# Kernel optimization log

Hardware: AMD Instinct MI355X
Metric: run time of the kernel (lower is better)

Reference implementation:

```python
import jax, jax.numpy as jnp
from jax import lax
import numpy as np

B, N = 8, 16384
C = 16            # layer_channels
K = 2             # kernel_size
L = 30            # layer_nums (layer 0 is plain causal conv, 29 gated layers)
AGG = 64          # agregate1x1 out channels
OUT = 256         # output1x1 out channels (8-bit classes)


def causal_conv(x, w, dilation):
    # x: (B, Cin, N), w: (Cout, Cin, K) -> (B, Cout, N), left-padded (causal)
    k = w.shape[-1]
    return lax.conv_general_dilated(
        x, w, window_strides=(1,), padding=[(dilation * (k - 1), 0)],
        rhs_dilation=(dilation,), dimension_numbers=('NCH', 'OIH', 'NCH'))


def setup_inputs() -> dict:
    key = jax.random.key(0)
    ks = jax.random.split(key, 16)
    s = 0.1
    x = jax.random.normal(ks[0], (B, N), dtype=jnp.float32) * 8000.0  # raw 16-bit-ish audio
    lengths = jax.random.randint(ks[1], (B,), N // 2, N, dtype=jnp.int32)
    return {
        'x': x,
        'lengths': lengths,
        'W0': jax.random.normal(ks[2], (C, 1, K), dtype=jnp.float32) * s,
        'b0': jnp.zeros((C,), dtype=jnp.float32),
        'Wf': jax.random.normal(ks[3], (L - 1, C, C, K), dtype=jnp.float32) * s,
        'bf': jnp.zeros((L - 1, C), dtype=jnp.float32),
        'Wg': jax.random.normal(ks[4], (L - 1, C, C, K), dtype=jnp.float32) * s,
        'bg': jnp.zeros((L - 1, C), dtype=jnp.float32),
        'Wr': jax.random.normal(ks[5], (L - 1, C, C), dtype=jnp.float32) * s,
        'br': jnp.zeros((L - 1, C), dtype=jnp.float32),
        'Wa': jax.random.normal(ks[6], (AGG, C), dtype=jnp.float32) * s,
        'ba': jnp.zeros((AGG,), dtype=jnp.float32),
        'Wo': jax.random.normal(ks[7], (OUT, AGG), dtype=jnp.float32) * s,
        'bo': jnp.zeros((OUT,), dtype=jnp.float32),
    }


def reference(x, lengths, W0, b0, Wf, bf, Wg, bg, Wr, br, Wa, ba, Wo, bo):
    inp = (x / 32768.0)[:, None, :]                     # (B,1,N), 65536/2 scaling
    # layer 0: plain causal conv 1 -> C
    h = causal_conv(inp, W0, 1) + b0[:, None]           # (B,C,N)
    skip = h
    inp = inp + h                                       # (B,1,N)+(B,C,N) broadcast
    for i in range(1, L):
        d = 2 ** (i % 10)
        j = i - 1
        f = jnp.tanh(causal_conv(inp, Wf[j], d) + bf[j][:, None])
        g = jax.nn.sigmoid(causal_conv(inp, Wg[j], d) + bg[j][:, None])
        z = f * g                                       # gated activation
        out = jnp.einsum('oc,bcn->bon', Wr[j], z) + br[j][:, None]
        skip = skip + out                               # skip-sum accumulation
        inp = inp + out                                 # residual
    a = jnp.einsum('oc,bcn->bon', Wa, jax.nn.relu(skip)) + ba[:, None]
    o = jnp.einsum('oc,bcn->bon', Wo, jax.nn.relu(a)) + bo[:, None]
    logp = jax.nn.log_softmax(o, axis=1)                # (B,OUT,N)
    mask = (jnp.arange(N) < lengths[:, None])[:, None, :].astype(logp.dtype)
    return logp * mask
```

## Files before the change

kernel.cpp:

```cpp
#include <hip/hip_runtime.h>
#include <hip/hip_bf16.h>

#define NN 16384
#define NC 16
#define NPOSTOT 131072
#define NLAY 29
#define TOUT 256
#define LSTR 24

typedef float4 f4;
typedef short bf16x8 __attribute__((ext_vector_type(8)));
typedef float f32x4 __attribute__((ext_vector_type(4)));

#define OFF_WF 0
#define OFF_WG (NLAY * 512)
#define OFF_WR (2 * NLAY * 512)
#define OFF_WA (3 * NLAY * 512)
#define OFF_WO (3 * NLAY * 512 + 2048)
#define PK_TOT (OFF_WO + 16384)

static __device__ __forceinline__ short to_bf16(float f) {
    __hip_bfloat16 h = __float2bfloat16(f);
    short s;
    __builtin_memcpy(&s, &h, 2);
    return s;
}
static __device__ __forceinline__ float from_bf16(short s) {
    unsigned int u = ((unsigned int)(unsigned short)s) << 16;
    float f;
    __builtin_memcpy(&f, &u, 4);
    return f;
}

__global__ __launch_bounds__(256) void prepack_k(
    const float* __restrict__ Wf, const float* __restrict__ Wg,
    const float* __restrict__ Wr, const float* __restrict__ Wa,
    const float* __restrict__ Wo, short* __restrict__ pk)
{
    const int i = blockIdx.x * 256 + threadIdx.x;
    if (i >= PK_TOT) return;
    float val;
    if (i < OFF_WG) {
        const int j = i >> 9, r = i & 511, l = r >> 3, j8 = r & 7;
        const int o = l & 15, h = l >> 4;
        const int k = h * 8 + j8, tap = k >> 4, c = k & 15;
        val = Wf[((j * 16 + o) * 16 + c) * 2 + tap];
    } else if (i < OFF_WA) {
        const int i2 = i - OFF_WG;
        if (i2 < NLAY * 512) {
            const int j = i2 >> 9, r = i2 & 511, l = r >> 3, j8 = r & 7;
            const int o = l & 15, h = l >> 4;
            const int k = h * 8 + j8, tap = k >> 4, c = k & 15;
            val = Wg[((j * 16 + o) * 16 + c) * 2 + tap];
        } else {
            const int i3 = i2 - NLAY * 512;
            const int j = i3 >> 9, r = i3 & 511, l = r >> 3, j8 = r & 7;
            const int o = l & 15, h = l >> 4;
            val = (j8 < 4) ? Wr[j * 256 + o * 16 + h * 4 + j8] : 0.0f;
        }
    } else if (i < OFF_WO) {
        const int i2 = i - OFF_WA;
        const int mt = i2 >> 9, r = i2 & 511, l = r >> 3, j8 = r & 7;
        const int og = mt * 16 + (l & 15), h = l >> 4;
        const int k = h * 8 + j8;
        val = (k < 16) ? Wa[og * 16 + k] : 0.0f;
    } else {
        const int i2 = i - OFF_WO;
        const int qt = i2 >> 10, hf = (i2 >> 9) & 1, r = i2 & 511;
        const int l = r >> 3, j8 = r & 7;
        const int q = qt * 16 + (l & 15), h = l >> 4;
        const int kg = hf * 32 + (j8 >> 2) * 16 + h * 4 + (j8 & 3);
        val = Wo[q * 64 + kg];
    }
    pk[i] = to_bf16(val);
}

static __device__ __forceinline__ f32x4 gated_core2(
    bf16x8 bx, bf16x8 af_, bf16x8 ag_, bf16x8 ar_,
    f32x4 cf, f32x4 cg, f32x4 cr)
{
    const f32x4 fp = __builtin_amdgcn_mfma_f32_16x16x32_bf16(af_, bx, cf, 0, 0, 0);
    const f32x4 gp = __builtin_amdgcn_mfma_f32_16x16x32_bf16(ag_, bx, cg, 0, 0, 0);

    bf16x8 bz;
#pragma unroll
    for (int r = 0; r < 4; ++r) {
        const float ef = __expf(2.0f * fminf(fp[r], 43.0f));
        const float eg = __expf(-gp[r]);
        const float den = fmaf(ef, eg, ef) + (eg + 1.0f);
        bz[r] = to_bf16((ef - 1.0f) * __builtin_amdgcn_rcpf(den));
        bz[r + 4] = 0;
    }
    return __builtin_amdgcn_mfma_f32_16x16x32_bf16(ar_, bz, cr, 0, 0, 0);
}

struct SegCfg { int d[8]; int nl; int jbase; int H; int l0; };

constexpr SegCfg CFGS[6] = {
    {{2, 4, 8, 16, 32, 64, 0, 0},     6, 0,  128, 1},
    {{128, 256, 0, 0, 0, 0, 0, 0},    2, 6,  256, 0},
    {{512, 1, 2, 4, 8, 16, 32, 64},   8, 8,  128, 0},
    {{128, 256, 0, 0, 0, 0, 0, 0},    2, 16, 256, 0},
    {{512, 1, 2, 4, 8, 16, 32, 64},   8, 18, 128, 0},
    {{128, 0, 0, 0, 0, 0, 0, 0},      1, 26, 0,   0},
};

template<int KI>
__global__ __launch_bounds__((TOUT + CFGS[KI].H) * 2)
void fused_t(const short* __restrict__ src, const float* __restrict__ x,
             const float* __restrict__ W0, const float* __restrict__ b0,
             short* __restrict__ dst, const short* __restrict__ pk,
             const float* __restrict__ bfA, const float* __restrict__ bgA,
             const float* __restrict__ brA)
{
    constexpr SegCfg cfg = CFGS[KI];
    constexpr int H = cfg.H;
    constexpr int Wp = TOUT + H;
    constexpr bool MULTI = (cfg.nl > 1);
    constexpr int LDSSZ = MULTI ? 2 * Wp * LSTR : 8;
    __shared__ short lds[LDSSZ];
    short* ldsA = lds;
    short* ldsB = lds + (MULTI ? Wp * LSTR : 0);

    const int t = threadIdx.x, lane = t & 63, wv = t >> 6;
    const int h = lane >> 4, i16 = lane & 15;
    const int tap = h >> 1, c0 = (h & 1) * 8;
    const int pbase = blockIdx.x * TOUT;
    const int bb = pbase >> 14, n0 = pbase & (NN - 1);
    const float* xrow = x + (size_t)bb * NN;
    const short* srow = src + (size_t)bb * NN * NC;

    const int l0r = wv * 32 + i16;
    const int l1r = l0r + 16;
    const int nA = n0 - H + l0r;
    const int nB = nA + 16;

    f32x4 res0, res1;

    {
        constexpr int d = cfg.d[0];
        constexpr int j = cfg.jbase;
        const bf16x8 af = *(const bf16x8*)(pk + OFF_WF + j * 512 + lane * 8);
        const bf16x8 ag = *(const bf16x8*)(pk + OFF_WG + j * 512 + lane * 8);
        const bf16x8 ar = *(const bf16x8*)(pk + OFF_WR + j * 512 + lane * 8);
        const f4 v1 = *(const f4*)(bfA + j * 16 + h * 4);
        const f4 v2 = *(const f4*)(bgA + j * 16 + h * 4);
        const f4 v3 = *(const f4*)(brA + j * 16 + h * 4);
        const f32x4 cf = {v1.x, v1.y, v1.z, v1.w};
        const f32x4 cg = {v2.x, v2.y, v2.z, v2.w};
        const f32x4 cr = {v3.x, v3.y, v3.z, v3.w};

        auto tile0 = [&](int l, int n, f32x4& res) {
            const int ns = tap ? n : n - d;
            bf16x8 bx = {0, 0, 0, 0, 0, 0, 0, 0};
            if (cfg.l0) {
                if (ns >= 0) {
                    const float xs = xrow[ns] * (1.0f / 32768.0f);
                    const float xm = (ns >= 1) ? xrow[ns - 1] * (1.0f / 32768.0f) : 0.0f;
#pragma unroll
                    for (int q2 = 0; q2 < 8; ++q2) {
                        const int c = c0 + q2;
                        bx[q2] = to_bf16(xs + fmaf(W0[c * 2], xm,
                                          fmaf(W0[c * 2 + 1], xs, b0[c])));
                    }
                }
            } else {
                if (ns >= 0) bx = *(const bf16x8*)(srow + (size_t)ns * NC + c0);
            }
            const f32x4 o = gated_core2(bx, af, ag, ar, cf, cg, cr);

            float r0, r1, r2, r3;
            if (cfg.l0) {
                if (n >= 0) {
                    const float xs = xrow[n] * (1.0f / 32768.0f);
                    const float xm = (n >= 1) ? xrow[n - 1] * (1.0f / 32768.0f) : 0.0f;
                    const int c = h * 4;
                    r0 = xs + fmaf(W0[c * 2 + 0], xm, fmaf(W0[c * 2 + 1], xs, b0[c + 0]));
                    r1 = xs + fmaf(W0[c * 2 + 2], xm, fmaf(W0[c * 2 + 3], xs, b0[c + 1]));
                    r2 = xs + fmaf(W0[c * 2 + 4], xm, fmaf(W0[c * 2 + 5], xs, b0[c + 2]));
                    r3 = xs + fmaf(W0[c * 2 + 6], xm, fmaf(W0[c * 2 + 7], xs, b0[c + 3]));
                } else { r0 = r1 = r2 = r3 = 0.0f; }
            } else {
                if (n >= 0) {
                    const short4 ov = *(const short4*)(srow + (size_t)n * NC + h * 4);
                    r0 = from_bf16(ov.x); r1 = from_bf16(ov.y);
                    r2 = from_bf16(ov.z); r3 = from_bf16(ov.w);
                } else { r0 = r1 = r2 = r3 = 0.0f; }
            }
            res[0] = r0 + o[0]; res[1] = r1 + o[1];
            res[2] = r2 + o[2]; res[3] = r3 + o[3];
            if (MULTI) {
                *(short4*)(ldsA + l * LSTR + h * 4) =
                    make_short4(to_bf16(res[0]), to_bf16(res[1]),
                                to_bf16(res[2]), to_bf16(res[3]));
            }
        };
        tile0(l0r, nA, res0);
        tile0(l1r, nB, res1);
    }
    if (MULTI) __syncthreads();

    int cur = 0;
#pragma unroll
    for (int s = 1; s < cfg.nl; ++s) {
        const int d = cfg.d[s];
        const int j = cfg.jbase + s;
        const bf16x8 af = *(const bf16x8*)(pk + OFF_WF + j * 512 + lane * 8);
        const bf16x8 ag = *(const bf16x8*)(pk + OFF_WG + j * 512 + lane * 8);
        const bf16x8 ar = *(const bf16x8*)(pk + OFF_WR + j * 512 + lane * 8);
        const f4 v1 = *(const f4*)(bfA + j * 16 + h * 4);
        const f4 v2 = *(const f4*)(bgA + j * 16 + h * 4);
        const f4 v3 = *(const f4*)(brA + j * 16 + h * 4);
        const f32x4 cf = {v1.x, v1.y, v1.z, v1.w};
        const f32x4 cg = {v2.x, v2.y, v2.z, v2.w};
        const f32x4 cr = {v3.x, v3.y, v3.z, v3.w};
        const short* rb = cur ? ldsB : ldsA;
        short* wb = cur ? ldsA : ldsB;
        const bool wr = (s + 1 < cfg.nl);

        auto tileL = [&](int l, int n, f32x4& res) {
            const int nt = tap ? n : n - d;
            int lt = tap ? l : l - d;
            if (lt < 0) lt = 0;
            bf16x8 bx = {0, 0, 0, 0, 0, 0, 0, 0};
            if (nt >= 0) bx = *(const bf16x8*)(rb + lt * LSTR + c0);
            const f32x4 o = gated_core2(bx, af, ag, ar, cf, cg, cr);
            res[0] += o[0]; res[1] += o[1]; res[2] += o[2]; res[3] += o[3];
            if (wr) {
                *(short4*)(wb + l * LSTR + h * 4) =
                    make_short4(to_bf16(res[0]), to_bf16(res[1]),
                                to_bf16(res[2]), to_bf16(res[3]));
            }
        };
        tileL(l0r, nA, res0);
        tileL(l1r, nB, res1);
        if (s + 1 < cfg.nl) __syncthreads();
        cur ^= 1;
    }

    if (l0r >= H) {
        *(short4*)(dst + ((size_t)bb * NN + nA) * NC + h * 4) =
            make_short4(to_bf16(res0[0]), to_bf16(res0[1]),
                        to_bf16(res0[2]), to_bf16(res0[3]));
    }
    if (l1r >= H) {
        *(short4*)(dst + ((size_t)bb * NN + nB) * NC + h * 4) =
            make_short4(to_bf16(res1[0]), to_bf16(res1[1]),
                        to_bf16(res1[2]), to_bf16(res1[3]));
    }
}

__global__ __launch_bounds__(512, 2) void headm_k(
    const short* __restrict__ src, const float* __restrict__ x,
    const int* __restrict__ lengths, const short* __restrict__ pk,
    const float* __restrict__ bfL, const float* __restrict__ bgL,
    const float* __restrict__ brL,
    const short* __restrict__ pka, const float* __restrict__ ba,
    const short* __restrict__ pko, const float* __restrict__ bo,
    float* __restrict__ out)
{
    __shared__ short ldsW[16384];
    __shared__ short ldsS0[8][256];
    __shared__ short ldsS1[8][256];
    __shared__ short ldsS2[8][256];

    const int t = threadIdx.x;
    const int lane = t & 63;
    const int wv = t >> 6;
    const int i16 = lane & 15;
    const int h = lane >> 4;
    const int pos = blockIdx.x * 128 + wv * 16 + i16;
    const int b = pos >> 14;
    const int n = pos & (NN - 1);
    const int tap = h >> 1, c0 = (h & 1) * 8;
    const short* srow = src + (size_t)b * NN * NC;

#pragma unroll
    for (int i = 0; i < 4; ++i)
        ((f4*)ldsW)[t + i * 512] = ((const f4*)pko)[t + i * 512];

    f32x4 r27n;
    {
        constexpr int j = NLAY - 2;
        const bf16x8 af = *(const bf16x8*)(pk + OFF_WF + j * 512 + lane * 8);
        const bf16x8 ag = *(const bf16x8*)(pk + OFF_WG + j * 512 + lane * 8);
        const bf16x8 ar = *(const bf16x8*)(pk + OFF_WR + j * 512 + lane * 8);
        const f4 v1 = *(const f4*)(bfL + j * 16 + h * 4);
        const f4 v2 = *(const f4*)(bgL + j * 16 + h * 4);
        const f4 v3 = *(const f4*)(brL + j * 16 + h * 4);
        const f32x4 cf = {v1.x, v1.y, v1.z, v1.w};
        const f32x4 cg = {v2.x, v2.y, v2.z, v2.w};
        const f32x4 cr = {v3.x, v3.y, v3.z, v3.w};

        auto run27 = [&](int p, short* dstS) -> f32x4 {
            const int ns = tap ? p : p - 256;
            bf16x8 bx = {0, 0, 0, 0, 0, 0, 0, 0};
            if (ns >= 0) bx = *(const bf16x8*)(srow + (size_t)ns * NC + c0);
            const f32x4 o = gated_core2(bx, af, ag, ar, cf, cg, cr);
            const short4 ov = *(const short4*)(srow + (size_t)p * NC + h * 4);
            f32x4 r;
            r[0] = from_bf16(ov.x) + o[0]; r[1] = from_bf16(ov.y) + o[1];
            r[2] = from_bf16(ov.z) + o[2]; r[3] = from_bf16(ov.w) + o[3];
            *(short4*)(dstS + i16 * 16 + h * 4) =
                make_short4(to_bf16(r[0]), to_bf16(r[1]),
                            to_bf16(r[2]), to_bf16(r[3]));
            return r;
        };
        r27n = run27(n, &ldsS0[wv][0]);
        if (n >= 512) run27(n - 512, &ldsS1[wv][0]);
    }

    {
        constexpr int j = NLAY - 1;
        const bf16x8 af = *(const bf16x8*)(pk + OFF_WF + j * 512 + lane * 8);
        const bf16x8 ag = *(const bf16x8*)(pk + OFF_WG + j * 512 + lane * 8);
        const bf16x8 ar = *(const bf16x8*)(pk + OFF_WR + j * 512 + lane * 8);
        const f4 v1 = *(const f4*)(bfL + j * 16 + h * 4);
        const f4 v2 = *(const f4*)(bgL + j * 16 + h * 4);
        const f4 v3 = *(const f4*)(brL + j * 16 + h * 4);
        const f32x4 cf = {v1.x, v1.y, v1.z, v1.w};
        const f32x4 cg = {v2.x, v2.y, v2.z, v2.w};
        const f32x4 cr = {v3.x, v3.y, v3.z, v3.w};

        bf16x8 bx = {0, 0, 0, 0, 0, 0, 0, 0};
        if (tap) {
            bx = *(const bf16x8*)(&ldsS0[wv][i16 * 16 + c0]);
        } else if (n >= 512) {
            bx = *(const bf16x8*)(&ldsS1[wv][i16 * 16 + c0]);
        }
        const f32x4 o = gated_core2(bx, af, ag, ar, cf, cg, cr);

        const float xs = x[pos] * (1.0f / 32768.0f);
        *(short4*)(&ldsS2[wv][i16 * 16 + h * 4]) = make_short4(
            to_bf16(fmaxf(r27n[0] + o[0] - xs, 0.0f)),
            to_bf16(fmaxf(r27n[1] + o[1] - xs, 0.0f)),
            to_bf16(fmaxf(r27n[2] + o[2] - xs, 0.0f)),
            to_bf16(fmaxf(r27n[3] + o[3] - xs, 0.0f)));
    }

    bf16x8 bs;
    if (h < 2) {
        bs = *(const bf16x8*)(&ldsS2[wv][i16 * 16 + h * 8]);
    } else {
#pragma unroll
        for (int j = 0; j < 8; ++j) bs[j] = 0;
    }

    float ra[16];
#pragma unroll
    for (int mt = 0; mt < 4; ++mt) {
        const bf16x8 aa = *(const bf16x8*)(pka + (mt * 64 + lane) * 8);
        const f4 bav = *(const f4*)(ba + mt * 16 + h * 4);
        f32x4 c = {bav.x, bav.y, bav.z, bav.w};
        c = __builtin_amdgcn_mfma_f32_16x16x32_bf16(aa, bs, c, 0, 0, 0);
#pragma unroll
        for (int r = 0; r < 4; ++r) ra[mt * 4 + r] = fmaxf(c[r], 0.0f);
    }
    bf16x8 blo, bhi;
#pragma unroll
    for (int j = 0; j < 8; ++j) { blo[j] = to_bf16(ra[j]); bhi[j] = to_bf16(ra[8 + j]); }

    __syncthreads();

    float lg[64];
#pragma unroll
    for (int qt = 0; qt < 16; ++qt) {
        const bf16x8 a0 = *(const bf16x8*)(ldsW + ((qt * 2 + 0) * 64 + lane) * 8);
        const bf16x8 a1 = *(const bf16x8*)(ldsW + ((qt * 2 + 1) * 64 + lane) * 8);
        const f4 bov = *(const f4*)(bo + qt * 16 + h * 4);
        f32x4 c = {bov.x, bov.y, bov.z, bov.w};
        c = __builtin_amdgcn_mfma_f32_16x16x32_bf16(a0, blo, c, 0, 0, 0);
        c = __builtin_amdgcn_mfma_f32_16x16x32_bf16(a1, bhi, c, 0, 0, 0);
#pragma unroll
        for (int r = 0; r < 4; ++r) lg[qt * 4 + r] = c[r];
    }

    float m = lg[0];
#pragma unroll
    for (int j = 1; j < 64; ++j) m = fmaxf(m, lg[j]);
    m = fmaxf(m, __shfl_xor(m, 16, 64));
    m = fmaxf(m, __shfl_xor(m, 32, 64));
    float s = 0.0f;
#pragma unroll
    for (int j = 0; j < 64; ++j) s += __expf(lg[j] - m);
    s += __shfl_xor(s, 16, 64);
    s += __shfl_xor(s, 32, 64);
    const float lse = m + __logf(s);
    const bool valid = n < lengths[b];

    float* ob = out + (size_t)b * 256 * NN + n;
#pragma unroll
    for (int qt = 0; qt < 16; ++qt)
#pragma unroll
        for (int r = 0; r < 4; ++r)
            ob[(size_t)(qt * 16 + h * 4 + r) * NN] = valid ? (lg[qt * 4 + r] - lse) : 0.0f;
}

extern "C" void kernel_launch(void* const* d_in, const int* in_sizes, int n_in,
                              void* d_out, int out_size, void* d_ws, size_t ws_size,
                              hipStream_t stream)
{
    const float* x       = (const float*)d_in[0];
    const int*   lengths = (const int*)d_in[1];
    const float* W0      = (const float*)d_in[2];
    const float* b0      = (const float*)d_in[3];
    const float* Wf      = (const float*)d_in[4];
    const float* bf      = (const float*)d_in[5];
    const float* Wg      = (const float*)d_in[6];
    const float* bg      = (const float*)d_in[7];
    const float* Wr      = (const float*)d_in[8];
    const float* br      = (const float*)d_in[9];
    const float* Wa      = (const float*)d_in[10];
    const float* ba      = (const float*)d_in[11];
    const float* Wo      = (const float*)d_in[12];
    const float* bo      = (const float*)d_in[13];
    float* out = (float*)d_out;

    short* bufA = (short*)d_ws;
    short* bufB = bufA + (size_t)NPOSTOT * NC;
    short* pk   = bufB + (size_t)NPOSTOT * NC;

    prepack_k<<<dim3((PK_TOT + 255) / 256), dim3(256), 0, stream>>>(
        Wf, Wg, Wr, Wa, Wo, pk);

#define FUSED(K, SRC, DST)                                                     \
    fused_t<K><<<dim3(NPOSTOT / TOUT), dim3((TOUT + CFGS[K].H) * 2), 0,        \
                 stream>>>(SRC, x, W0, b0, DST, pk, bf, bg, br)

    FUSED(0, bufA, bufA);
    FUSED(1, bufA, bufB);
    FUSED(2, bufB, bufA);
    FUSED(3, bufA, bufB);
    FUSED(4, bufB, bufA);
    FUSED(5, bufA, bufB);
#undef FUSED

    headm_k<<<dim3(NPOSTOT / 128), dim3(512), 0, stream>>>(
        bufB, x, lengths, pk, bf, bg, br,
        pk + OFF_WA, ba, pk + OFF_WO, bo, out);
}
```

Baseline: 132.4 us.

## Fold layer 26 into head kernel and drop the separate single-layer launch

```diff
diff --git a/kernel.cpp b/kernel.cpp
--- a/kernel.cpp
+++ b/kernel.cpp
@@ -96,13 +96,12 @@
 
 struct SegCfg { int d[8]; int nl; int jbase; int H; int l0; };
 
-constexpr SegCfg CFGS[6] = {
+constexpr SegCfg CFGS[5] = {
     {{2, 4, 8, 16, 32, 64, 0, 0},     6, 0,  128, 1},
     {{128, 256, 0, 0, 0, 0, 0, 0},    2, 6,  256, 0},
     {{512, 1, 2, 4, 8, 16, 32, 64},   8, 8,  128, 0},
     {{128, 256, 0, 0, 0, 0, 0, 0},    2, 16, 256, 0},
     {{512, 1, 2, 4, 8, 16, 32, 64},   8, 18, 128, 0},
-    {{128, 0, 0, 0, 0, 0, 0, 0},      1, 26, 0,   0},
 };
 
 template<int KI>
@@ -260,9 +259,9 @@
     float* __restrict__ out)
 {
     __shared__ short ldsW[16384];
-    __shared__ short ldsS0[8][256];
-    __shared__ short ldsS1[8][256];
-    __shared__ short ldsS2[8][256];
+    __shared__ short S26[4][8][256];
+    __shared__ short S27[2][8][256];
+    __shared__ short SK[8][256];
 
     const int t = threadIdx.x;
     const int lane = t & 63;
@@ -278,6 +277,39 @@
 #pragma unroll
     for (int i = 0; i < 4; ++i)
         ((f4*)ldsW)[t + i * 512] = ((const f4*)pko)[t + i * 512];
+
+    f32x4 r26a, r26c;
+    {
+        constexpr int j = NLAY - 3;
+        const bf16x8 af = *(const bf16x8*)(pk + OFF_WF + j * 512 + lane * 8);
+        const bf16x8 ag = *(const bf16x8*)(pk + OFF_WG + j * 512 + lane * 8);
+        const bf16x8 ar = *(const bf16x8*)(pk + OFF_WR + j * 512 + lane * 8);
+        const f4 v1 = *(const f4*)(bfL + j * 16 + h * 4);
+        const f4 v2 = *(const f4*)(bgL + j * 16 + h * 4);
+        const f4 v3 = *(const f4*)(brL + j * 16 + h * 4);
+        const f32x4 cf = {v1.x, v1.y, v1.z, v1.w};
+        const f32x4 cg = {v2.x, v2.y, v2.z, v2.w};
+        const f32x4 cr = {v3.x, v3.y, v3.z, v3.w};
+
+        auto run26 = [&](int p, short* dstS) -> f32x4 {
+            const int ns = tap ? p : p - 128;
+            bf16x8 bx = {0, 0, 0, 0, 0, 0, 0, 0};
+            if (ns >= 0) bx = *(const bf16x8*)(srow + (size_t)ns * NC + c0);
+            const f32x4 o = gated_core2(bx, af, ag, ar, cf, cg, cr);
+            const short4 ov = *(const short4*)(srow + (size_t)p * NC + h * 4);
+            f32x4 r;
+            r[0] = from_bf16(ov.x) + o[0]; r[1] = from_bf16(ov.y) + o[1];
+            r[2] = from_bf16(ov.z) + o[2]; r[3] = from_bf16(ov.w) + o[3];
+            *(short4*)(dstS + i16 * 16 + h * 4) =
+                make_short4(to_bf16(r[0]), to_bf16(r[1]),
+                            to_bf16(r[2]), to_bf16(r[3]));
+            return r;
+        };
+        r26a = run26(n, &S26[0][wv][0]);
+        if (n >= 256) run26(n - 256, &S26[1][wv][0]);
+        if (n >= 512) r26c = run26(n - 512, &S26[2][wv][0]);
+        if (n >= 768) run26(n - 768, &S26[3][wv][0]);
+    }
 
     f32x4 r27n;
     {
@@ -292,22 +324,26 @@
         const f32x4 cg = {v2.x, v2.y, v2.z, v2.w};
         const f32x4 cr = {v3.x, v3.y, v3.z, v3.w};
 
-        auto run27 = [&](int p, short* dstS) -> f32x4 {
-            const int ns = tap ? p : p - 256;
+        {
             bf16x8 bx = {0, 0, 0, 0, 0, 0, 0, 0};
-            if (ns >= 0) bx = *(const bf16x8*)(srow + (size_t)ns * NC + c0);
+            if (tap) bx = *(const bf16x8*)(&S26[0][wv][i16 * 16 + c0]);
+            else if (n >= 256) bx = *(const bf16x8*)(&S26[1][wv][i16 * 16 + c0]);
             const f32x4 o = gated_core2(bx, af, ag, ar, cf, cg, cr);
-            const short4 ov = *(const short4*)(srow + (size_t)p * NC + h * 4);
-            f32x4 r;
-            r[0] = from_bf16(ov.x) + o[0]; r[1] = from_bf16(ov.y) + o[1];
-            r[2] = from_bf16(ov.z) + o[2]; r[3] = from_bf16(ov.w) + o[3];
-            *(short4*)(dstS + i16 * 16 + h * 4) =
-                make_short4(to_bf16(r[0]), to_bf16(r[1]),
-                            to_bf16(r[2]), to_bf16(r[3]));
-            return r;
-        };
-        r27n = run27(n, &ldsS0[wv][0]);
-        if (n >= 512) run27(n - 512, &ldsS1[wv][0]);
+            r27n[0] = r26a[0] + o[0]; r27n[1] = r26a[1] + o[1];
+            r27n[2] = r26a[2] + o[2]; r27n[3] = r26a[3] + o[3];
+            *(short4*)(&S27[0][wv][i16 * 16 + h * 4]) =
+                make_short4(to_bf16(r27n[0]), to_bf16(r27n[1]),
+                            to_bf16(r27n[2]), to_bf16(r27n[3]));
+        }
+        if (n >= 512) {
+            bf16x8 bx = {0, 0, 0, 0, 0, 0, 0, 0};
+            if (tap) bx = *(const bf16x8*)(&S26[2][wv][i16 * 16 + c0]);
+            else if (n >= 768) bx = *(const bf16x8*)(&S26[3][wv][i16 * 16 + c0]);
+            const f32x4 o = gated_core2(bx, af, ag, ar, cf, cg, cr);
+            *(short4*)(&S27[1][wv][i16 * 16 + h * 4]) = make_short4(
+                to_bf16(r26c[0] + o[0]), to_bf16(r26c[1] + o[1]),
+                to_bf16(r26c[2] + o[2]), to_bf16(r26c[3] + o[3]));
+        }
     }
 
     {
@@ -323,15 +359,12 @@
         const f32x4 cr = {v3.x, v3.y, v3.z, v3.w};
 
         bf16x8 bx = {0, 0, 0, 0, 0, 0, 0, 0};
-        if (tap) {
-            bx = *(const bf16x8*)(&ldsS0[wv][i16 * 16 + c0]);
-        } else if (n >= 512) {
-            bx = *(const bf16x8*)(&ldsS1[wv][i16 * 16 + c0]);
-        }
+        if (tap) bx = *(const bf16x8*)(&S27[0][wv][i16 * 16 + c0]);
+        else if (n >= 512) bx = *(const bf16x8*)(&S27[1][wv][i16 * 16 + c0]);
         const f32x4 o = gated_core2(bx, af, ag, ar, cf, cg, cr);
 
         const float xs = x[pos] * (1.0f / 32768.0f);
-        *(short4*)(&ldsS2[wv][i16 * 16 + h * 4]) = make_short4(
+        *(short4*)(&SK[wv][i16 * 16 + h * 4]) = make_short4(
             to_bf16(fmaxf(r27n[0] + o[0] - xs, 0.0f)),
             to_bf16(fmaxf(r27n[1] + o[1] - xs, 0.0f)),
             to_bf16(fmaxf(r27n[2] + o[2] - xs, 0.0f)),
@@ -340,7 +373,7 @@
 
     bf16x8 bs;
     if (h < 2) {
-        bs = *(const bf16x8*)(&ldsS2[wv][i16 * 16 + h * 8]);
+        bs = *(const bf16x8*)(&SK[wv][i16 * 16 + h * 8]);
     } else {
 #pragma unroll
         for (int j = 0; j < 8; ++j) bs[j] = 0;
@@ -432,10 +465,9 @@
     FUSED(2, bufB, bufA);
     FUSED(3, bufA, bufB);
     FUSED(4, bufB, bufA);
-    FUSED(5, bufA, bufB);
 #undef FUSED
 
     headm_k<<<dim3(NPOSTOT / 128), dim3(512), 0, stream>>>(
-        bufB, x, lengths, pk, bf, bg, br,
+        bufA, x, lengths, pk, bf, bg, br,
         pk + OFF_WA, ba, pk + OFF_WO, bo, out);
 }
```

Result: no change. 130.9 us, median of 2 (-1.2%).
